# Optimization experiments

Measured on AMD Instinct MI355X. Metric: run time of the kernel, lower is better.

## Reference

```python
import jax, jax.numpy as jnp
import numpy as np

NUM_STEPS = 8  # fixed-step RK4 stand-in for adaptive DormandPrince(atol=1e-5)
B, D, C, H = 8192, 508, 1, 256
DIN = D + C + 1  # state + conditional + time


def _mlp(h, w0, b0, w1, b1, w2, b2):
    h = jnp.tanh(h @ w0 + b0)
    h = jnp.tanh(h @ w1 + b1)
    return h @ w2 + b2


def setup_inputs() -> dict:
    key = jax.random.key(0)
    ks = jax.random.split(key, 6)
    sc = lambda k, shape, fan: jax.random.normal(k, shape, jnp.float32) / np.sqrt(fan)
    return {
        "x": jax.random.normal(ks[0], (B, D), jnp.float32),
        "cond": jax.random.uniform(ks[1], (B, C), jnp.float32),
        "eps": jax.random.normal(ks[2], (B, D), jnp.float32),  # Hutchinson probe
        "w0": sc(ks[3], (DIN, H), DIN),
        "b0": jnp.zeros((H,), jnp.float32),
        "w1": sc(ks[4], (H, H), H),
        "b1": jnp.zeros((H,), jnp.float32),
        "w2": sc(ks[5], (H, D), H),
        "b2": jnp.zeros((D,), jnp.float32),
    }


def reference(x, cond, eps, w0, b0, w1, b1, w2, b2):
    """FFJORD bijector forward: integrate dx/dt = f(t, x, cond) from t=0 to 1
    with augmented Hutchinson trace estimate d(logdet)/dt = eps^T (df/dx) eps.
    Returns (y, log_det_jacobian_estimate)."""
    dt = jnp.float32(1.0 / NUM_STEPS)

    def dyn(t, y):
        def f(y_):
            tcol = jnp.full((y_.shape[0], 1), t, y_.dtype)
            return _mlp(jnp.concatenate([y_, cond, tcol], axis=-1),
                        w0, b0, w1, b1, w2, b2)
        fy, vjp_fn = jax.vjp(f, y)
        (etJ,) = vjp_fn(eps)           # eps^T J
        tr = jnp.sum(etJ * eps, -1)    # eps^T J eps  -> [B]
        return fy, tr

    def step(carry, i):
        y, ld = carry
        t = i * dt
        k1, l1 = dyn(t, y)
        k2, l2 = dyn(t + 0.5 * dt, y + 0.5 * dt * k1)
        k3, l3 = dyn(t + 0.5 * dt, y + 0.5 * dt * k2)
        k4, l4 = dyn(t + dt, y + dt * k3)
        y = y + (dt / 6.0) * (k1 + 2.0 * k2 + 2.0 * k3 + k4)
        ld = ld + (dt / 6.0) * (l1 + 2.0 * l2 + 2.0 * l3 + l4)
        return (y, ld), None

    init = (x, jnp.zeros((x.shape[0],), x.dtype))
    (y, ld), _ = jax.lax.scan(step, init, jnp.arange(NUM_STEPS, dtype=x.dtype))
    return y, ld
```

## Files before the change

### kernel.cpp

```cpp
#include <hip/hip_runtime.h>
#include <math.h>

namespace {

constexpr int Bn = 8192;
constexpr int Dn = 508;
constexpr int Hn = 256;
constexpr int NSTEPS = 8;
constexpr int Kp = 512;
constexpr float DT = 1.f / NSTEPS;
constexpr float DT6 = DT / 6.f;

typedef __attribute__((ext_vector_type(8))) short short8v;
typedef __attribute__((ext_vector_type(4))) float f32x4;

__device__ __forceinline__ short f2b(float f) {
  union { float f; unsigned u; } v; v.f = f;
  unsigned r = v.u + 0x7fffu + ((v.u >> 16) & 1u);
  return (short)(r >> 16);
}
__device__ __forceinline__ float b2f(short s) {
  union { unsigned u; float f; } v;
  v.u = ((unsigned)(unsigned short)s) << 16;
  return v.f;
}
__device__ __forceinline__ unsigned pk2(short lo, short hi) {
  return ((unsigned)(unsigned short)lo) | (((unsigned)(unsigned short)hi) << 16);
}
__device__ __forceinline__ float upk_lo(unsigned p) {
  union { unsigned u; float f; } v; v.u = p << 16; return v.f;
}
__device__ __forceinline__ float upk_hi(unsigned p) {
  union { unsigned u; float f; } v; v.u = p & 0xffff0000u; return v.f;
}
__device__ __forceinline__ float ftanh(float x) {
  x = fminf(fmaxf(x, -12.f), 12.f);
  const float e = __expf(2.f * x);
  return __fdividef(e - 1.f, e + 1.f);
}

template <int KT>
__device__ __forceinline__ void gemm_bb(const short* __restrict__ A, int lda,
                                        const short* __restrict__ Bt, int ldb,
                                        int row0, int col0, int lane,
                                        f32x4 acc[2][2]) {
  const int r = lane & 15, g = lane >> 4;
  const short* a0p = A + (size_t)(row0 + r) * lda + g * 8;
  const short* a1p = A + (size_t)(row0 + 16 + r) * lda + g * 8;
  const short* b0p = Bt + (size_t)(col0 + r) * ldb + g * 8;
  const short* b1p = Bt + (size_t)(col0 + 16 + r) * ldb + g * 8;
#pragma unroll
  for (int kt = 0; kt < KT; ++kt) {
    const short8v a0 = *(const short8v*)(a0p + kt * 32);
    const short8v a1 = *(const short8v*)(a1p + kt * 32);
    const short8v b0 = *(const short8v*)(b0p + kt * 32);
    const short8v b1 = *(const short8v*)(b1p + kt * 32);
    acc[0][0] = __builtin_amdgcn_mfma_f32_16x16x32_bf16(a0, b0, acc[0][0], 0, 0, 0);
    acc[0][1] = __builtin_amdgcn_mfma_f32_16x16x32_bf16(a0, b1, acc[0][1], 0, 0, 0);
    acc[1][0] = __builtin_amdgcn_mfma_f32_16x16x32_bf16(a1, b0, acc[1][0], 0, 0, 0);
    acc[1][1] = __builtin_amdgcn_mfma_f32_16x16x32_bf16(a1, b1, acc[1][1], 0, 0, 0);
  }
}

#define GEMM_PROLOGUE()                                     \
  const int tid = threadIdx.x, wid = tid >> 6, lane = tid & 63; \
  const int row0 = blockIdx.y * 64 + (wid >> 1) * 32;       \
  const int col0 = blockIdx.x * 64 + (wid & 1) * 32;        \
  const int rq = (lane >> 4) * 4, cc = lane & 15;           \
  const f32x4 z4 = {0.f, 0.f, 0.f, 0.f};                    \
  f32x4 acc[2][2] = {{z4, z4}, {z4, z4}};


__global__ __launch_bounds__(256) void k_cast_bf(const float* __restrict__ src, int R,
                                                 int C, short* __restrict__ dst, int ldd) {
  const int total = R * ldd;
  for (int idx = blockIdx.x * 256 + threadIdx.x; idx < total; idx += gridDim.x * 256) {
    const int r = idx / ldd, c = idx - r * ldd;
    dst[idx] = (c < C) ? f2b(src[(size_t)r * C + c]) : (short)0;
  }
}

__global__ __launch_bounds__(256) void k_transpose_bf(const float* __restrict__ src, int K,
                                                      int N, short* __restrict__ dst,
                                                      int Nd, int ldd) {
  const int total = Nd * ldd;
  for (int idx = blockIdx.x * 256 + threadIdx.x; idx < total; idx += gridDim.x * 256) {
    const int n = idx / ldd, k = idx - n * ldd;
    dst[idx] = (k < K && n < N) ? f2b(src[(size_t)k * N + n]) : (short)0;
  }
}

__global__ __launch_bounds__(256) void k_c0(const float* __restrict__ w0,
                                            const float* __restrict__ b2,
                                            float* __restrict__ c0) {
  const int n = threadIdx.x;
  float s = 0.f;
#pragma unroll 8
  for (int d = 0; d < Dn; ++d) s += b2[d] * w0[(size_t)d * Hn + n];
  c0[n] = s;
}

__global__ __launch_bounds__(256) void k_w20t(const short* __restrict__ w0T,
                                              const short* __restrict__ w2b,
                                              short* __restrict__ w20T) {
  GEMM_PROLOGUE();
  gemm_bb<16>(w0T, Kp, w2b, Kp, row0, col0, lane, acc);
#pragma unroll
  for (int i = 0; i < 2; ++i)
#pragma unroll
    for (int j = 0; j < 2; ++j)
#pragma unroll
      for (int q = 0; q < 4; ++q)
        w20T[(size_t)(row0 + i * 16 + rq + q) * Hn + col0 + j * 16 + cc] =
            f2b(acc[i][j][q]);
}

template <int MODE>
__global__ __launch_bounds__(256) void k_ginit(const short* __restrict__ A,
                                               const short* __restrict__ Bt,
                                               const float* __restrict__ cond,
                                               const float* __restrict__ w0c,
                                               float* __restrict__ zout,
                                               short* __restrict__ bout) {
  GEMM_PROLOGUE();
  gemm_bb<16>(A, Kp, Bt, Kp, row0, col0, lane, acc);
#pragma unroll
  for (int i = 0; i < 2; ++i)
#pragma unroll
    for (int j = 0; j < 2; ++j)
#pragma unroll
      for (int q = 0; q < 4; ++q) {
        const int row = row0 + i * 16 + rq + q;
        const int col = col0 + j * 16 + cc;
        const size_t idx = (size_t)row * Hn + col;
        if (MODE == 0)
          zout[idx] = acc[i][j][q] + cond[row] * w0c[col];
        else
          bout[idx] = f2b(acc[i][j][q]);
      }
}

__global__ __launch_bounds__(256) void k_fragpack(const short* __restrict__ src,
                                                  short* __restrict__ dst, int total) {
  for (int idx = blockIdx.x * 256 + threadIdx.x; idx < total; idx += gridDim.x * 256) {
    const int j = idx & 7;
    const int l = (idx >> 3) & 63;
    const int ks = (idx >> 9) & 7;
    const int c16 = idx >> 12;
    dst[idx] = src[(size_t)(c16 * 16 + (l & 15)) * 256 + ks * 32 + (l >> 4) * 8 + j];
  }
}


__device__ __forceinline__ int swz(int row, int col) {
  return (row * 256 + col) ^ ((row & 7) << 3);
}

__global__ __launch_bounds__(512) void k_mega(
    const float* __restrict__ zg, const short* __restrict__ u_g,
    const short* __restrict__ g2_g, const short* __restrict__ w1P,
    const short* __restrict__ w20P, const short* __restrict__ w2P,
    const float* __restrict__ b0, const float* __restrict__ w0t,
    const float* __restrict__ b1, const float* __restrict__ c0,
    const float* __restrict__ b2, const float* __restrict__ x,
    float* __restrict__ yout, float* __restrict__ ldout) {
  __shared__ short As[32 * 256];
  __shared__ short h1s[16 * 256];
  __shared__ float red[16][8];

  const int tid = threadIdx.x;
  const int w = tid >> 6, lane = tid & 63;
  const int cc = lane & 15, g = lane >> 4, rq = g * 4;
  const int r0 = blockIdx.x * 16;
  const int cb = w * 32;

  float b0c[2], w0tc[2], b1c[2], c0c[2];
#pragma unroll
  for (int nt = 0; nt < 2; ++nt) {
    const int col = cb + nt * 16 + cc;
    b0c[nt] = b0[col];
    w0tc[nt] = w0t[col];
    b1c[nt] = b1[col];
    c0c[nt] = c0[col];
  }

  const short* w1base = w1P + (size_t)(2 * w) * 4096 + lane * 8;
  const short* w20base = w20P + (size_t)(2 * w) * 4096 + lane * 8;

  const size_t gbase = (size_t)(r0 + rq) * Hn + cb + cc;

  float z_[2][4], kzp[2][4], kza[2][4], hs[2][4], tr_[4];
  unsigned u_pk[2][2], g2_pk[2][2];
#pragma unroll
  for (int nt = 0; nt < 2; ++nt) {
    const size_t i0 = gbase + nt * 16;
#pragma unroll
    for (int q = 0; q < 4; ++q) {
      z_[nt][q] = zg[i0 + (size_t)q * Hn];
      kzp[nt][q] = 0.f;
      hs[nt][q] = 0.f;
    }
    u_pk[nt][0] = pk2(u_g[i0], u_g[i0 + Hn]);
    u_pk[nt][1] = pk2(u_g[i0 + 2 * Hn], u_g[i0 + 3 * Hn]);
    g2_pk[nt][0] = pk2(g2_g[i0], g2_g[i0 + Hn]);
    g2_pk[nt][1] = pk2(g2_g[i0 + 2 * Hn], g2_g[i0 + 3 * Hn]);
  }
#pragma unroll
  for (int q = 0; q < 4; ++q) tr_[q] = 0.f;

  const f32x4 zero4 = {0.f, 0.f, 0.f, 0.f};

#pragma unroll 1
  for (int e = 0; e < 4 * NSTEPS; ++e) {
    const int j = e & 3, s = e >> 2;
    const float oj = (j == 0) ? 0.f : ((j == 3) ? 1.f : 0.5f);
    const float aj = (j == 0) ? 0.f : ((j == 3) ? DT : 0.5f * DT);
    const float mj = (j == 1 || j == 2) ? 2.f : 1.f;
    const float tval = ((float)s + oj) * DT;

#pragma unroll
    for (int nt = 0; nt < 2; ++nt)
#pragma unroll
      for (int q = 0; q < 4; ++q) {
        const int row = rq + q;
        const int colh = cb + nt * 16 + cc;
        const float pre = z_[nt][q] + aj * kzp[nt][q] + b0c[nt] + tval * w0tc[nt];
        const float h = ftanh(pre);
        const float uq = (q & 1) ? upk_hi(u_pk[nt][q >> 1]) : upk_lo(u_pk[nt][q >> 1]);
        As[swz(row, colh)] = f2b(h);
        As[swz(16 + row, colh)] = f2b((1.f - h * h) * uq);
      }
    __syncthreads();

    {
      f32x4 acc[2][2] = {{zero4, zero4}, {zero4, zero4}};
#pragma unroll
      for (int ks = 0; ks < 8; ++ks) {
        const short8v b0v = *(const short8v*)(w1base + ks * 512);
        const short8v b1v = *(const short8v*)(w1base + 4096 + ks * 512);
        const short8v a0 = *(const short8v*)(As + swz(cc, g * 8 + ks * 32));
        const short8v a1 = *(const short8v*)(As + swz(16 + cc, g * 8 + ks * 32));
        acc[0][0] = __builtin_amdgcn_mfma_f32_16x16x32_bf16(a0, b0v, acc[0][0], 0, 0, 0);
        acc[0][1] = __builtin_amdgcn_mfma_f32_16x16x32_bf16(a0, b1v, acc[0][1], 0, 0, 0);
        acc[1][0] = __builtin_amdgcn_mfma_f32_16x16x32_bf16(a1, b0v, acc[1][0], 0, 0, 0);
        acc[1][1] = __builtin_amdgcn_mfma_f32_16x16x32_bf16(a1, b1v, acc[1][1], 0, 0, 0);
      }
#pragma unroll
      for (int nt = 0; nt < 2; ++nt)
#pragma unroll
        for (int q = 0; q < 4; ++q) {
          const float v = ftanh(acc[0][nt][q] + b1c[nt]);
          const float g2q =
              (q & 1) ? upk_hi(g2_pk[nt][q >> 1]) : upk_lo(g2_pk[nt][q >> 1]);
          tr_[q] += (DT6 * mj) * g2q * (1.f - v * v) * acc[1][nt][q];
          h1s[swz(rq + q, cb + nt * 16 + cc)] = f2b(v);
          hs[nt][q] += mj * v;
        }
    }
    __syncthreads();

    {
      f32x4 acc2[2] = {zero4, zero4};
#pragma unroll
      for (int ks = 0; ks < 8; ++ks) {
        const short8v b0v = *(const short8v*)(w20base + ks * 512);
        const short8v b1v = *(const short8v*)(w20base + 4096 + ks * 512);
        const short8v a = *(const short8v*)(h1s + swz(cc, g * 8 + ks * 32));
        acc2[0] = __builtin_amdgcn_mfma_f32_16x16x32_bf16(a, b0v, acc2[0], 0, 0, 0);
        acc2[1] = __builtin_amdgcn_mfma_f32_16x16x32_bf16(a, b1v, acc2[1], 0, 0, 0);
      }
#pragma unroll
      for (int nt = 0; nt < 2; ++nt)
#pragma unroll
        for (int q = 0; q < 4; ++q) {
          const float kzv = acc2[nt][q] + c0c[nt];
          if (j == 0) {
            kza[nt][q] = kzv;
            kzp[nt][q] = kzv;
          } else if (j < 3) {
            kza[nt][q] += mj * kzv;
            kzp[nt][q] = kzv;
          } else {
            z_[nt][q] += DT6 * (kza[nt][q] + kzv);
          }
        }
    }
  }

#pragma unroll
  for (int nt = 0; nt < 2; ++nt)
#pragma unroll
    for (int q = 0; q < 4; ++q)
      As[swz(rq + q, cb + nt * 16 + cc)] = f2b(hs[nt][q]);
  __syncthreads();
  {
    const short* w2base = w2P + (size_t)(4 * w) * 4096 + lane * 8;
    f32x4 facc[4] = {zero4, zero4, zero4, zero4};
#pragma unroll
    for (int ks = 0; ks < 8; ++ks) {
      const short8v a = *(const short8v*)(As + swz(cc, g * 8 + ks * 32));
#pragma unroll
      for (int nt = 0; nt < 4; ++nt) {
        const short8v bv = *(const short8v*)(w2base + nt * 4096 + ks * 512);
        facc[nt] = __builtin_amdgcn_mfma_f32_16x16x32_bf16(a, bv, facc[nt], 0, 0, 0);
      }
    }
#pragma unroll
    for (int nt = 0; nt < 4; ++nt) {
      const int colo = w * 64 + nt * 16 + cc;
      if (colo < Dn) {
        const float b2c = b2[colo];
#pragma unroll
        for (int q = 0; q < 4; ++q) {
          const size_t ix = (size_t)(r0 + rq + q) * Dn + colo;
          yout[ix] = x[ix] + DT6 * facc[nt][q] + b2c;
        }
      }
    }
  }

#pragma unroll
  for (int q = 0; q < 4; ++q) {
    float v = tr_[q];
    v += __shfl_xor(v, 1);
    v += __shfl_xor(v, 2);
    v += __shfl_xor(v, 4);
    v += __shfl_xor(v, 8);
    if (cc == 0) red[rq + q][w] = v;
  }
  __syncthreads();
  if (tid < 16) {
    float t = 0.f;
#pragma unroll
    for (int ww = 0; ww < 8; ++ww) t += red[tid][ww];
    ldout[r0 + tid] = t;
  }
}

}

extern "C" void kernel_launch(void* const* d_in, const int* in_sizes, int n_in,
                              void* d_out, int out_size, void* d_ws, size_t ws_size,
                              hipStream_t stream) {
  const float* x = (const float*)d_in[0];
  const float* cond = (const float*)d_in[1];
  const float* eps = (const float*)d_in[2];
  const float* w0 = (const float*)d_in[3];
  const float* b0 = (const float*)d_in[4];
  const float* w1 = (const float*)d_in[5];
  const float* b1 = (const float*)d_in[6];
  const float* w2 = (const float*)d_in[7];
  const float* b2 = (const float*)d_in[8];
  const float* w0c = w0 + (size_t)508 * Hn;
  const float* w0t = w0 + (size_t)509 * Hn;

  const size_t BD = (size_t)Bn * Dn, BH = (size_t)Bn * Hn, BKp = (size_t)Bn * Kp;
  char* p = (char*)d_ws;
  auto alloc_f = [&](size_t n) { float* r = (float*)p; p += n * 4; return r; };
  auto alloc_s = [&](size_t n) { short* r = (short*)p; p += ((n * 2 + 15) & ~15ull); return r; };

  float* zg = alloc_f(BH);
  float* c0 = alloc_f(256);
  short* xp = alloc_s(BKp);
  short* epsp = alloc_s(BKp);
  short* u_g = alloc_s(BH);
  short* g2_g = alloc_s(BH);
  short* w0T = alloc_s(256 * 512);
  short* w1T = alloc_s(256 * 256);
  short* w2b = alloc_s(256 * 512);
  short* w2T = alloc_s(512 * 256);
  short* w20T = alloc_s(256 * 256);
  short* w1P = alloc_s(256 * 256);
  short* w20P = alloc_s(256 * 256);
  short* w2P = alloc_s(512 * 256);

  float* yout = (float*)d_out;
  float* ldout = (float*)d_out + BD;

  const dim3 blk(256);
  const dim3 gH(Hn / 64, Bn / 64);
  const dim3 gW(4, 4);

  k_cast_bf<<<4096, blk, 0, stream>>>(x, Bn, Dn, xp, Kp);
  k_cast_bf<<<4096, blk, 0, stream>>>(eps, Bn, Dn, epsp, Kp);
  k_cast_bf<<<512, blk, 0, stream>>>(w2, Hn, Dn, w2b, Kp);
  k_transpose_bf<<<256, blk, 0, stream>>>(w1, Hn, Hn, w1T, Hn, Hn);
  k_transpose_bf<<<512, blk, 0, stream>>>(w0, Dn, Hn, w0T, Hn, Kp);
  k_transpose_bf<<<512, blk, 0, stream>>>(w2, Hn, Dn, w2T, Kp, Hn);
  k_c0<<<1, blk, 0, stream>>>(w0, b2, c0);
  k_w20t<<<gW, blk, 0, stream>>>(w0T, w2b, w20T);
  k_ginit<0><<<gH, blk, 0, stream>>>(xp, w0T, cond, w0c, zg, nullptr);
  k_ginit<1><<<gH, blk, 0, stream>>>(epsp, w0T, nullptr, nullptr, nullptr, u_g);
  k_ginit<2><<<gH, blk, 0, stream>>>(epsp, w2b, nullptr, nullptr, nullptr, g2_g);
  k_fragpack<<<256, blk, 0, stream>>>(w1T, w1P, 256 * 256);
  k_fragpack<<<256, blk, 0, stream>>>(w20T, w20P, 256 * 256);
  k_fragpack<<<512, blk, 0, stream>>>(w2T, w2P, 512 * 256);

  k_mega<<<dim3(Bn / 16), dim3(512), 0, stream>>>(zg, u_g, g2_g, w1P, w20P,
                                                  w2P, b0, w0t, b1, c0, b2, x,
                                                  yout, ldout);
}
```

Baseline: 323.1 us.

## Fuse fp32-to-bf16 input casts into init GEMMs and cut mega-kernel register pressure

```diff
diff --git a/kernel.cpp b/kernel.cpp
--- a/kernel.cpp
+++ b/kernel.cpp
@@ -116,14 +116,43 @@
 }
 
 template <int MODE>
-__global__ __launch_bounds__(256) void k_ginit(const short* __restrict__ A,
-                                               const short* __restrict__ Bt,
-                                               const float* __restrict__ cond,
-                                               const float* __restrict__ w0c,
-                                               float* __restrict__ zout,
-                                               short* __restrict__ bout) {
+__global__ __launch_bounds__(256) void k_ginit32(const float* __restrict__ Af,
+                                                 const short* __restrict__ Bt,
+                                                 const float* __restrict__ cond,
+                                                 const float* __restrict__ w0c,
+                                                 float* __restrict__ zout,
+                                                 short* __restrict__ bout) {
   GEMM_PROLOGUE();
-  gemm_bb<16>(A, Kp, Bt, Kp, row0, col0, lane, acc);
+  const int g = lane >> 4;
+  const float* a0r = Af + (size_t)(row0 + cc) * Dn;
+  const float* a1r = Af + (size_t)(row0 + 16 + cc) * Dn;
+  const short* b0p = Bt + (size_t)(col0 + cc) * Kp + g * 8;
+  const short* b1p = Bt + (size_t)(col0 + 16 + cc) * Kp + g * 8;
+#pragma unroll
+  for (int kt = 0; kt < 16; ++kt) {
+    const int k = kt * 32 + g * 8;
+    short8v a0v, a1v;
+#pragma unroll
+    for (int h = 0; h < 2; ++h) {
+      const int k4 = k + h * 4;
+      float4 fa = make_float4(0.f, 0.f, 0.f, 0.f);
+      float4 fb = make_float4(0.f, 0.f, 0.f, 0.f);
+      if (k4 < Dn) {
+        fa = *(const float4*)(a0r + k4);
+        fb = *(const float4*)(a1r + k4);
+      }
+      a0v[h * 4 + 0] = f2b(fa.x); a0v[h * 4 + 1] = f2b(fa.y);
+      a0v[h * 4 + 2] = f2b(fa.z); a0v[h * 4 + 3] = f2b(fa.w);
+      a1v[h * 4 + 0] = f2b(fb.x); a1v[h * 4 + 1] = f2b(fb.y);
+      a1v[h * 4 + 2] = f2b(fb.z); a1v[h * 4 + 3] = f2b(fb.w);
+    }
+    const short8v b0v = *(const short8v*)(b0p + kt * 32);
+    const short8v b1v = *(const short8v*)(b1p + kt * 32);
+    acc[0][0] = __builtin_amdgcn_mfma_f32_16x16x32_bf16(a0v, b0v, acc[0][0], 0, 0, 0);
+    acc[0][1] = __builtin_amdgcn_mfma_f32_16x16x32_bf16(a0v, b1v, acc[0][1], 0, 0, 0);
+    acc[1][0] = __builtin_amdgcn_mfma_f32_16x16x32_bf16(a1v, b0v, acc[1][0], 0, 0, 0);
+    acc[1][1] = __builtin_amdgcn_mfma_f32_16x16x32_bf16(a1v, b1v, acc[1][1], 0, 0, 0);
+  }
 #pragma unroll
   for (int i = 0; i < 2; ++i)
 #pragma unroll
@@ -156,7 +185,10 @@
   return (row * 256 + col) ^ ((row & 7) << 3);
 }
 
-__global__ __launch_bounds__(512) void k_mega(
+constexpr int HP = 258;
+
+__global__ __launch_bounds__(512)
+__attribute__((amdgpu_waves_per_eu(4))) void k_mega(
     const float* __restrict__ zg, const short* __restrict__ u_g,
     const short* __restrict__ g2_g, const short* __restrict__ w1P,
     const short* __restrict__ w20P, const short* __restrict__ w2P,
@@ -166,6 +198,7 @@
     float* __restrict__ yout, float* __restrict__ ldout) {
   __shared__ short As[32 * 256];
   __shared__ short h1s[16 * 256];
+  __shared__ float hsum[16 * HP];
   __shared__ float red[16][8];
 
   const int tid = threadIdx.x;
@@ -189,7 +222,7 @@
 
   const size_t gbase = (size_t)(r0 + rq) * Hn + cb + cc;
 
-  float z_[2][4], kzp[2][4], kza[2][4], hs[2][4], tr_[4];
+  float z_[2][4], kzp[2][4], kza[2][4], tr_[4];
   unsigned u_pk[2][2], g2_pk[2][2];
 #pragma unroll
   for (int nt = 0; nt < 2; ++nt) {
@@ -198,7 +231,6 @@
     for (int q = 0; q < 4; ++q) {
       z_[nt][q] = zg[i0 + (size_t)q * Hn];
       kzp[nt][q] = 0.f;
-      hs[nt][q] = 0.f;
     }
     u_pk[nt][0] = pk2(u_g[i0], u_g[i0 + Hn]);
     u_pk[nt][1] = pk2(u_g[i0 + 2 * Hn], u_g[i0 + 3 * Hn]);
@@ -207,6 +239,8 @@
   }
 #pragma unroll
   for (int q = 0; q < 4; ++q) tr_[q] = 0.f;
+
+  for (int i = tid; i < 16 * HP; i += 512) hsum[i] = 0.f;
 
   const f32x4 zero4 = {0.f, 0.f, 0.f, 0.f};
 
@@ -232,35 +266,36 @@
       }
     __syncthreads();
 
-    {
-      f32x4 acc[2][2] = {{zero4, zero4}, {zero4, zero4}};
+#pragma unroll
+    for (int nt = 0; nt < 2; ++nt) {
+      f32x4 aH = zero4, aM = zero4;
+      __builtin_amdgcn_s_setprio(1);
 #pragma unroll
       for (int ks = 0; ks < 8; ++ks) {
-        const short8v b0v = *(const short8v*)(w1base + ks * 512);
-        const short8v b1v = *(const short8v*)(w1base + 4096 + ks * 512);
+        const short8v bv = *(const short8v*)(w1base + nt * 4096 + ks * 512);
         const short8v a0 = *(const short8v*)(As + swz(cc, g * 8 + ks * 32));
         const short8v a1 = *(const short8v*)(As + swz(16 + cc, g * 8 + ks * 32));
-        acc[0][0] = __builtin_amdgcn_mfma_f32_16x16x32_bf16(a0, b0v, acc[0][0], 0, 0, 0);
-        acc[0][1] = __builtin_amdgcn_mfma_f32_16x16x32_bf16(a0, b1v, acc[0][1], 0, 0, 0);
-        acc[1][0] = __builtin_amdgcn_mfma_f32_16x16x32_bf16(a1, b0v, acc[1][0], 0, 0, 0);
-        acc[1][1] = __builtin_amdgcn_mfma_f32_16x16x32_bf16(a1, b1v, acc[1][1], 0, 0, 0);
-      }
-#pragma unroll
-      for (int nt = 0; nt < 2; ++nt)
-#pragma unroll
-        for (int q = 0; q < 4; ++q) {
-          const float v = ftanh(acc[0][nt][q] + b1c[nt]);
-          const float g2q =
-              (q & 1) ? upk_hi(g2_pk[nt][q >> 1]) : upk_lo(g2_pk[nt][q >> 1]);
-          tr_[q] += (DT6 * mj) * g2q * (1.f - v * v) * acc[1][nt][q];
-          h1s[swz(rq + q, cb + nt * 16 + cc)] = f2b(v);
-          hs[nt][q] += mj * v;
-        }
+        aH = __builtin_amdgcn_mfma_f32_16x16x32_bf16(a0, bv, aH, 0, 0, 0);
+        aM = __builtin_amdgcn_mfma_f32_16x16x32_bf16(a1, bv, aM, 0, 0, 0);
+      }
+      __builtin_amdgcn_s_setprio(0);
+#pragma unroll
+      for (int q = 0; q < 4; ++q) {
+        const float v = ftanh(aH[q] + b1c[nt]);
+        const float g2q =
+            (q & 1) ? upk_hi(g2_pk[nt][q >> 1]) : upk_lo(g2_pk[nt][q >> 1]);
+        tr_[q] += (DT6 * mj) * g2q * (1.f - v * v) * aM[q];
+        const int row = rq + q;
+        const int colh = cb + nt * 16 + cc;
+        h1s[swz(row, colh)] = f2b(v);
+        hsum[row * HP + colh] += mj * v;
+      }
     }
     __syncthreads();
 
     {
       f32x4 acc2[2] = {zero4, zero4};
+      __builtin_amdgcn_s_setprio(1);
 #pragma unroll
       for (int ks = 0; ks < 8; ++ks) {
         const short8v b0v = *(const short8v*)(w20base + ks * 512);
@@ -269,6 +304,7 @@
         acc2[0] = __builtin_amdgcn_mfma_f32_16x16x32_bf16(a, b0v, acc2[0], 0, 0, 0);
         acc2[1] = __builtin_amdgcn_mfma_f32_16x16x32_bf16(a, b1v, acc2[1], 0, 0, 0);
       }
+      __builtin_amdgcn_s_setprio(0);
 #pragma unroll
       for (int nt = 0; nt < 2; ++nt)
 #pragma unroll
@@ -290,12 +326,16 @@
 #pragma unroll
   for (int nt = 0; nt < 2; ++nt)
 #pragma unroll
-    for (int q = 0; q < 4; ++q)
-      As[swz(rq + q, cb + nt * 16 + cc)] = f2b(hs[nt][q]);
+    for (int q = 0; q < 4; ++q) {
+      const int row = rq + q;
+      const int colh = cb + nt * 16 + cc;
+      As[swz(row, colh)] = f2b(hsum[row * HP + colh]);
+    }
   __syncthreads();
   {
     const short* w2base = w2P + (size_t)(4 * w) * 4096 + lane * 8;
     f32x4 facc[4] = {zero4, zero4, zero4, zero4};
+    __builtin_amdgcn_s_setprio(1);
 #pragma unroll
     for (int ks = 0; ks < 8; ++ks) {
       const short8v a = *(const short8v*)(As + swz(cc, g * 8 + ks * 32));
@@ -305,6 +345,7 @@
         facc[nt] = __builtin_amdgcn_mfma_f32_16x16x32_bf16(a, bv, facc[nt], 0, 0, 0);
       }
     }
+    __builtin_amdgcn_s_setprio(0);
 #pragma unroll
     for (int nt = 0; nt < 4; ++nt) {
       const int colo = w * 64 + nt * 16 + cc;
@@ -354,15 +395,13 @@
   const float* w0c = w0 + (size_t)508 * Hn;
   const float* w0t = w0 + (size_t)509 * Hn;
 
-  const size_t BD = (size_t)Bn * Dn, BH = (size_t)Bn * Hn, BKp = (size_t)Bn * Kp;
+  const size_t BD = (size_t)Bn * Dn, BH = (size_t)Bn * Hn;
   char* p = (char*)d_ws;
   auto alloc_f = [&](size_t n) { float* r = (float*)p; p += n * 4; return r; };
   auto alloc_s = [&](size_t n) { short* r = (short*)p; p += ((n * 2 + 15) & ~15ull); return r; };
 
   float* zg = alloc_f(BH);
   float* c0 = alloc_f(256);
-  short* xp = alloc_s(BKp);
-  short* epsp = alloc_s(BKp);
   short* u_g = alloc_s(BH);
   short* g2_g = alloc_s(BH);
   short* w0T = alloc_s(256 * 512);
@@ -381,17 +420,15 @@
   const dim3 gH(Hn / 64, Bn / 64);
   const dim3 gW(4, 4);
 
-  k_cast_bf<<<4096, blk, 0, stream>>>(x, Bn, Dn, xp, Kp);
-  k_cast_bf<<<4096, blk, 0, stream>>>(eps, Bn, Dn, epsp, Kp);
   k_cast_bf<<<512, blk, 0, stream>>>(w2, Hn, Dn, w2b, Kp);
   k_transpose_bf<<<256, blk, 0, stream>>>(w1, Hn, Hn, w1T, Hn, Hn);
   k_transpose_bf<<<512, blk, 0, stream>>>(w0, Dn, Hn, w0T, Hn, Kp);
   k_transpose_bf<<<512, blk, 0, stream>>>(w2, Hn, Dn, w2T, Kp, Hn);
   k_c0<<<1, blk, 0, stream>>>(w0, b2, c0);
   k_w20t<<<gW, blk, 0, stream>>>(w0T, w2b, w20T);
-  k_ginit<0><<<gH, blk, 0, stream>>>(xp, w0T, cond, w0c, zg, nullptr);
-  k_ginit<1><<<gH, blk, 0, stream>>>(epsp, w0T, nullptr, nullptr, nullptr, u_g);
-  k_ginit<2><<<gH, blk, 0, stream>>>(epsp, w2b, nullptr, nullptr, nullptr, g2_g);
+  k_ginit32<0><<<gH, blk, 0, stream>>>(x, w0T, cond, w0c, zg, nullptr);
+  k_ginit32<1><<<gH, blk, 0, stream>>>(eps, w0T, nullptr, nullptr, nullptr, u_g);
+  k_ginit32<2><<<gH, blk, 0, stream>>>(eps, w2b, nullptr, nullptr, nullptr, g2_g);
   k_fragpack<<<256, blk, 0, stream>>>(w1T, w1P, 256 * 256);
   k_fragpack<<<256, blk, 0, stream>>>(w20T, w20P, 256 * 256);
   k_fragpack<<<512, blk, 0, stream>>>(w2T, w2P, 512 * 256);
```

Result: slower. 1.209 ms (+274.2%).
